# Kernel tuning notes

Hardware: AMD Instinct MI355X
Metric: run time of the kernel (lower is better)

Reference implementation:

```python
import jax, jax.numpy as jnp
import numpy as np

B, T, D_IN, H = 1024, 512, 32, 64


def setup_inputs() -> dict:
    key = jax.random.key(0)
    ks = jax.random.split(key, 16)
    s_in = 1.0 / np.sqrt(H)  # torch LSTM init scale 1/sqrt(hidden)
    inp = {
        "x": jax.random.normal(ks[0], (B, T, D_IN), dtype=jnp.float32),
        # layer 0
        "Wih0": jax.random.uniform(ks[1], (4 * H, D_IN), minval=-s_in, maxval=s_in),
        "Whh0": jax.random.uniform(ks[2], (4 * H, H), minval=-s_in, maxval=s_in),
        "bih0": jax.random.uniform(ks[3], (4 * H,), minval=-s_in, maxval=s_in),
        "bhh0": jax.random.uniform(ks[4], (4 * H,), minval=-s_in, maxval=s_in),
        # layer 1
        "Wih1": jax.random.uniform(ks[5], (4 * H, H), minval=-s_in, maxval=s_in),
        "Whh1": jax.random.uniform(ks[6], (4 * H, H), minval=-s_in, maxval=s_in),
        "bih1": jax.random.uniform(ks[7], (4 * H,), minval=-s_in, maxval=s_in),
        "bhh1": jax.random.uniform(ks[8], (4 * H,), minval=-s_in, maxval=s_in),
        # head: Linear(H, H//2) -> ReLU -> Linear(H//2, 1)
        "W1": jax.random.uniform(ks[9], (H // 2, H), minval=-s_in, maxval=s_in),
        "b1": jax.random.uniform(ks[10], (H // 2,), minval=-s_in, maxval=s_in),
        "W2": jax.random.uniform(ks[11], (1, H // 2), minval=-1.0 / np.sqrt(H // 2), maxval=1.0 / np.sqrt(H // 2)),
        "b2": jax.random.uniform(ks[12], (1,), minval=-1.0 / np.sqrt(H // 2), maxval=1.0 / np.sqrt(H // 2)),
    }
    return inp


def _lstm_layer(x, Wih, Whh, bih, bhh):
    # x: [B, T, D]; returns all hidden states [B, T, H]
    b = x.shape[0]
    xT = jnp.swapaxes(x, 0, 1)  # [T, B, D]
    h0 = jnp.zeros((b, H), dtype=x.dtype)
    c0 = jnp.zeros((b, H), dtype=x.dtype)
    bias = bih + bhh

    def step(carry, xt):
        h, c = carry
        z = xt @ Wih.T + h @ Whh.T + bias  # [B, 4H]
        i, f, g, o = jnp.split(z, 4, axis=-1)  # torch gate order: i, f, g, o
        i = jax.nn.sigmoid(i)
        f = jax.nn.sigmoid(f)
        g = jnp.tanh(g)
        o = jax.nn.sigmoid(o)
        c = f * c + i * g
        h = o * jnp.tanh(c)
        return (h, c), h

    _, hs = jax.lax.scan(step, (h0, c0), xT)
    return jnp.swapaxes(hs, 0, 1)  # [B, T, H]


def reference(x, Wih0, Whh0, bih0, bhh0, Wih1, Whh1, bih1, bhh1, W1, b1, W2, b2):
    h1 = _lstm_layer(x, Wih0, Whh0, bih0, bhh0)   # [B, T, H]
    h2 = _lstm_layer(h1, Wih1, Whh1, bih1, bhh1)  # [B, T, H] (dropout = identity, eval)
    last = h2[:, -1]                              # [B, H]
    hidden = jax.nn.relu(last @ W1.T + b1)        # [B, H//2]
    out = hidden @ W2.T + b2                      # [B, 1]
    return out[:, 0]                              # [B]
```

## Files before the change

kernel.cpp:

```cpp
#include <hip/hip_runtime.h>

#define T       512
#define DIN     32
#define HCELLS  64
#define NB      16
#define NSLICE  64
#define TB      256
#define CH      16
#define NCH     (T / CH)

typedef _Float16 half8  __attribute__((ext_vector_type(8)));
typedef _Float16 half4v __attribute__((ext_vector_type(4)));
typedef float    float4v __attribute__((ext_vector_type(4)));

#define STRH    72
#define SB_HALFS (2*16*STRH)

#define LOG2E   1.44269504f
#define SLOG2E  2.88539008f

#define BARRIER() asm volatile("s_waitcnt lgkmcnt(0)\n\ts_barrier" ::: "memory")

#define WS_FLAG_BYTES 4096
#define H0T   (16 * HCELLS)
#define H0S   ((size_t)T * H0T)
#define WS_NEED (WS_FLAG_BYTES + (size_t)NSLICE * H0S * sizeof(_Float16))

__device__ __forceinline__ int hidx(int p, int n, int k) { return (p * 16 + n) * STRH + k; }

__device__ __forceinline__ void cvt8(const float* v, half8& hi) {
    #pragma unroll
    for (int e = 0; e < 8; ++e) hi[e] = (_Float16)v[e];
}

__device__ __forceinline__ void cell_vec(float4v z0, float4v z1, float4v z2, float4v z3,
                                         float4v& cs, half4v& hh, float4v* hout)
{
    float4v ei, ef, G2, eo, rFP, C2, rOC;
    #pragma unroll
    for (int r = 0; r < 4; ++r) ei[r] = __builtin_amdgcn_exp2f(z0[r]);
    #pragma unroll
    for (int r = 0; r < 4; ++r) ef[r] = __builtin_amdgcn_exp2f(z1[r]);
    #pragma unroll
    for (int r = 0; r < 4; ++r) G2[r] = __builtin_amdgcn_exp2f(z2[r]);
    #pragma unroll
    for (int r = 0; r < 4; ++r) eo[r] = __builtin_amdgcn_exp2f(z3[r]);

    float4v I  = 1.0f + ei;
    float4v F  = 1.0f + ef;
    float4v Gp = 1.0f + G2;
    float4v P  = I * Gp;
    float4v FP = F * P;
    #pragma unroll
    for (int r = 0; r < 4; ++r) rFP[r] = __builtin_amdgcn_rcpf(FP[r]);

    float4v Gms, num, csn;
    #pragma unroll
    for (int r = 0; r < 4; ++r) Gms[r] = fmaf(SLOG2E, G2[r], -SLOG2E);
    #pragma unroll
    for (int r = 0; r < 4; ++r) num[r] = fmaf(F[r], Gms[r], cs[r] * P[r]);
    csn = num * rFP;
    #pragma unroll
    for (int r = 0; r < 4; ++r) csn[r] = fminf(fmaxf(csn[r], -50.0f), 50.0f);
    cs = csn;

    #pragma unroll
    for (int r = 0; r < 4; ++r) C2[r] = __builtin_amdgcn_exp2f(csn[r]);
    float4v O   = 1.0f + eo;
    float4v OCp = O * (1.0f + C2);
    #pragma unroll
    for (int r = 0; r < 4; ++r) rOC[r] = __builtin_amdgcn_rcpf(OCp[r]);
    float4v h = (C2 - 1.0f) * rOC;
    if (hout) *hout = h;
    #pragma unroll
    for (int r = 0; r < 4; ++r) hh[r] = (_Float16)h[r];
}

__global__ void __launch_bounds__(TB, 1)
lstm2_pipe_kernel(const float* __restrict__ x,
                  const float* __restrict__ Wih0, const float* __restrict__ Whh0,
                  const float* __restrict__ bih0, const float* __restrict__ bhh0,
                  const float* __restrict__ Wih1, const float* __restrict__ Whh1,
                  const float* __restrict__ bih1, const float* __restrict__ bhh1,
                  const float* __restrict__ W1,   const float* __restrict__ b1,
                  const float* __restrict__ W2,   const float* __restrict__ b2,
                  unsigned* __restrict__ prog, _Float16* __restrict__ h0g,
                  float* __restrict__ out)
{
    const int tid  = threadIdx.x;
    const int wl   = tid >> 6;
    const int lane = tid & 63;
    const int n16  = lane & 15;
    const int q    = lane >> 4;
    const int j0   = wl * 16 + q * 4;

    const int g     = blockIdx.x;
    const int role  = (g >> 3) & 1;
    const int slice = ((g >> 4) << 3) | (g & 7);
    const int b0    = slice * NB;

    __shared__ __align__(16) _Float16 SB[SB_HALFS];
    __shared__ __align__(16) float HS[16 * 68 + 16 * 33];

    const float gsc[4] = {-LOG2E, -LOG2E, SLOG2E, -LOG2E};

    half8 ah[4][4];
    float4v biasv[4];

    #pragma unroll
    for (int l = 0; l < 4; ++l) {
        const int row = (l * 4 + wl) * 16 + n16;
        const float g2 = gsc[l];
        float v[8];
        if (role == 0) {
            {
                const float4* p = (const float4*)(Wih0 + row * DIN + q * 8);
                float4 u0 = p[0], u1 = p[1];
                v[0]=g2*u0.x; v[1]=g2*u0.y; v[2]=g2*u0.z; v[3]=g2*u0.w;
                v[4]=g2*u1.x; v[5]=g2*u1.y; v[6]=g2*u1.z; v[7]=g2*u1.w;
                cvt8(v, ah[l][0]);
            }
            #pragma unroll
            for (int kt = 1; kt < 3; ++kt) {
                const float4* p = (const float4*)(Whh0 + row * HCELLS + (kt - 1) * 32 + q * 8);
                float4 u0 = p[0], u1 = p[1];
                v[0]=g2*u0.x; v[1]=g2*u0.y; v[2]=g2*u0.z; v[3]=g2*u0.w;
                v[4]=g2*u1.x; v[5]=g2*u1.y; v[6]=g2*u1.z; v[7]=g2*u1.w;
                cvt8(v, ah[l][kt]);
            }
            const int r0 = l * 64 + j0;
            float4v bi = *(const float4v*)(bih0 + r0);
            float4v bh = *(const float4v*)(bhh0 + r0);
            biasv[l] = (bi + bh) * g2;
        } else {
            #pragma unroll
            for (int kt = 0; kt < 4; ++kt) {
                const float* base = (kt < 2) ? (Wih1 + row * HCELLS + kt * 32)
                                             : (Whh1 + row * HCELLS + (kt - 2) * 32);
                const float4* p = (const float4*)(base + q * 8);
                float4 u0 = p[0], u1 = p[1];
                v[0]=g2*u0.x; v[1]=g2*u0.y; v[2]=g2*u0.z; v[3]=g2*u0.w;
                v[4]=g2*u1.x; v[5]=g2*u1.y; v[6]=g2*u1.z; v[7]=g2*u1.w;
                cvt8(v, ah[l][kt]);
            }
            const int r0 = l * 64 + j0;
            float4v bi = *(const float4v*)(bih1 + r0);
            float4v bh = *(const float4v*)(bhh1 + r0);
            biasv[l] = (bi + bh) * g2;
        }
    }

    for (int i = tid; i < SB_HALFS / 2; i += TB) ((int*)SB)[i] = 0;
    __syncthreads();

    float4v cs4 = {0.f, 0.f, 0.f, 0.f};
    float4v hl4;

    if (role == 0) {
        const float* xq = x + ((size_t)(b0 + n16) * T) * DIN + q * 8;
        float4 xn0 = ((const float4*)xq)[0];
        float4 xn1 = ((const float4*)xq)[1];
        xq += DIN;

        _Float16* hstream = h0g + (size_t)slice * H0S + n16 * HCELLS + j0;

        #pragma unroll 2
        for (int t = 0; t < T; ++t) {
            const int pr = t & 1, pw = pr ^ 1;

            float4 xc0 = xn0, xc1 = xn1;
            if (t + 1 < T) { xn0 = ((const float4*)xq)[0]; xn1 = ((const float4*)xq)[1]; xq += DIN; }

            half8 bhx;
            bhx[0]=(_Float16)xc0.x; bhx[1]=(_Float16)xc0.y; bhx[2]=(_Float16)xc0.z; bhx[3]=(_Float16)xc0.w;
            bhx[4]=(_Float16)xc1.x; bhx[5]=(_Float16)xc1.y; bhx[6]=(_Float16)xc1.z; bhx[7]=(_Float16)xc1.w;

            float4v acc[4];
            #pragma unroll
            for (int l = 0; l < 4; ++l)
                acc[l] = __builtin_amdgcn_mfma_f32_16x16x32_f16(ah[l][0], bhx, biasv[l], 0, 0, 0);
            half8 bh0a = *(const half8*)&SB[hidx(pr, n16, q * 8)];
            half8 bh0b = *(const half8*)&SB[hidx(pr, n16, 32 + q * 8)];
            #pragma unroll
            for (int l = 0; l < 4; ++l)
                acc[l] = __builtin_amdgcn_mfma_f32_16x16x32_f16(ah[l][1], bh0a, acc[l], 0, 0, 0);
            #pragma unroll
            for (int l = 0; l < 4; ++l)
                acc[l] = __builtin_amdgcn_mfma_f32_16x16x32_f16(ah[l][2], bh0b, acc[l], 0, 0, 0);

            half4v hh;
            cell_vec(acc[0], acc[1], acc[2], acc[3], cs4, hh, nullptr);
            *(half4v*)&SB[hidx(pw, n16, j0)] = hh;
            *(half4v*)(hstream + (size_t)t * H0T) = hh;

            if ((t & (CH - 1)) == (CH - 1)) {
                __syncthreads();
                if (tid == 0)
                    __hip_atomic_store(prog + slice, (unsigned)(t / CH + 1),
                                       __ATOMIC_RELEASE, __HIP_MEMORY_SCOPE_AGENT);
            } else {
                BARRIER();
            }
        }
        return;
    }

    const _Float16* gbase = h0g + (size_t)slice * H0S + n16 * HCELLS;
    const int ka = q * 8, kb = 32 + q * 8;

    half8 a_cur, b_cur;
    for (int c = 0; c < NCH; ++c) {
        if (tid == 0) {
            unsigned v;
            while ((v = __hip_atomic_load(prog + slice, __ATOMIC_ACQUIRE,
                                          __HIP_MEMORY_SCOPE_AGENT)) < (unsigned)(c + 1))
                __builtin_amdgcn_s_sleep(2);
        }
        __syncthreads();

        {
            const _Float16* p0 = gbase + (size_t)(c * CH) * H0T;
            a_cur = *(const half8*)(p0 + ka);
            b_cur = *(const half8*)(p0 + kb);
        }

        #pragma unroll 2
        for (int i = 0; i < CH; ++i) {
            const int t = c * CH + i;
            const int sr = (i + 1) & 1;
            const int sw = i & 1;

            half8 a_nxt, b_nxt;
            if (i + 1 < CH) {
                const _Float16* pn = gbase + (size_t)(t + 1) * H0T;
                a_nxt = *(const half8*)(pn + ka);
                b_nxt = *(const half8*)(pn + kb);
            }

            float4v acc[4];
            #pragma unroll
            for (int l = 0; l < 4; ++l)
                acc[l] = __builtin_amdgcn_mfma_f32_16x16x32_f16(ah[l][0], a_cur, biasv[l], 0, 0, 0);
            #pragma unroll
            for (int l = 0; l < 4; ++l)
                acc[l] = __builtin_amdgcn_mfma_f32_16x16x32_f16(ah[l][1], b_cur, acc[l], 0, 0, 0);
            half8 c1 = *(const half8*)&SB[hidx(sr, n16, q * 8)];
            half8 c2 = *(const half8*)&SB[hidx(sr, n16, 32 + q * 8)];
            #pragma unroll
            for (int l = 0; l < 4; ++l)
                acc[l] = __builtin_amdgcn_mfma_f32_16x16x32_f16(ah[l][2], c1, acc[l], 0, 0, 0);
            #pragma unroll
            for (int l = 0; l < 4; ++l)
                acc[l] = __builtin_amdgcn_mfma_f32_16x16x32_f16(ah[l][3], c2, acc[l], 0, 0, 0);

            half4v hh;
            cell_vec(acc[0], acc[1], acc[2], acc[3], cs4, hh, &hl4);
            *(half4v*)&SB[hidx(sw, n16, j0)] = hh;
            BARRIER();

            a_cur = a_nxt; b_cur = b_nxt;
        }
    }

    float* h1f = HS;
    float* hid = HS + 16 * 68;
    *(float4v*)&h1f[n16 * 68 + j0] = hl4;
    __syncthreads();

    {
        const int n2 = tid >> 4, m = tid & 15;
        float s0 = b1[m], s1 = b1[m + 16];
        const float* w0p = W1 + m * HCELLS;
        const float* w1p = W1 + (m + 16) * HCELLS;
        #pragma unroll
        for (int j = 0; j < HCELLS; ++j) {
            float hv = h1f[n2 * 68 + j];
            s0 = fmaf(w0p[j], hv, s0);
            s1 = fmaf(w1p[j], hv, s1);
        }
        hid[n2 * 33 + m]      = fmaxf(s0, 0.0f);
        hid[n2 * 33 + m + 16] = fmaxf(s1, 0.0f);
    }
    __syncthreads();

    if (tid < NB) {
        float s = b2[0];
        #pragma unroll
        for (int m = 0; m < 32; ++m) s = fmaf(W2[m], hid[tid * 33 + m], s);
        out[b0 + tid] = s;
    }
}

#define TBF     512
#define FB_H0   0
#define FB_H1   (2*16*STRH)
#define FB_HALFS (FB_H1 + 2*16*STRH)

__device__ __forceinline__ void cell_update(const float4v acc[4], float* cs,
                                            half4v& hh, float* hout)
{
    #pragma unroll
    for (int r = 0; r < 4; ++r) {
        float ei = __builtin_amdgcn_exp2f(acc[0][r]);
        float ef = __builtin_amdgcn_exp2f(acc[1][r]);
        float G2 = __builtin_amdgcn_exp2f(acc[2][r]);
        float I  = 1.0f + ei, F = 1.0f + ef;
        float Gp = 1.0f + G2;
        float Gms = fmaf(SLOG2E, G2, -SLOG2E);
        float P   = I * Gp;
        float num = fmaf(F, Gms, cs[r] * P);
        float csn = num * __builtin_amdgcn_rcpf(F * P);
        csn = fminf(fmaxf(csn, -50.0f), 50.0f);
        cs[r] = csn;
        float eo = __builtin_amdgcn_exp2f(acc[3][r]);
        float C2 = __builtin_amdgcn_exp2f(csn);
        float O  = 1.0f + eo;
        float Cp = 1.0f + C2, Cm = C2 - 1.0f;
        float h  = Cm * __builtin_amdgcn_rcpf(O * Cp);
        if (hout) hout[r] = h;
        hh[r] = (_Float16)h;
    }
}

__global__ void __launch_bounds__(TBF, 2)
lstm2_mfma_fallback(const float* __restrict__ x,
                    const float* __restrict__ Wih0, const float* __restrict__ Whh0,
                    const float* __restrict__ bih0, const float* __restrict__ bhh0,
                    const float* __restrict__ Wih1, const float* __restrict__ Whh1,
                    const float* __restrict__ bih1, const float* __restrict__ bhh1,
                    const float* __restrict__ W1,   const float* __restrict__ b1,
                    const float* __restrict__ W2,   const float* __restrict__ b2,
                    float* __restrict__ out)
{
    const int tid  = threadIdx.x;
    const int wid  = tid >> 6;
    const int grp  = wid >> 2;
    const int wl   = wid & 3;
    const int lane = tid & 63;
    const int n16  = lane & 15;
    const int q    = lane >> 4;
    const int j0   = wl * 16 + q * 4;
    const int b0   = blockIdx.x * NB;

    __shared__ __align__(16) _Float16 SB[FB_HALFS];
    __shared__ __align__(16) float HS[16 * 68 + 16 * 33];

    const float gsc[4] = {-LOG2E, -LOG2E, SLOG2E, -LOG2E};
    half8 ah[4][4];
    float4v biasv[4];

    #pragma unroll
    for (int l = 0; l < 4; ++l) {
        const int row = (l * 4 + wl) * 16 + n16;
        const float g = gsc[l];
        float v[8];
        if (grp == 0) {
            {
                const float4* p = (const float4*)(Wih0 + row * DIN + q * 8);
                float4 u0 = p[0], u1 = p[1];
                v[0]=g*u0.x; v[1]=g*u0.y; v[2]=g*u0.z; v[3]=g*u0.w;
                v[4]=g*u1.x; v[5]=g*u1.y; v[6]=g*u1.z; v[7]=g*u1.w;
                cvt8(v, ah[l][0]);
            }
            #pragma unroll
            for (int kt = 1; kt < 3; ++kt) {
                const float4* p = (const float4*)(Whh0 + row * HCELLS + (kt - 1) * 32 + q * 8);
                float4 u0 = p[0], u1 = p[1];
                v[0]=g*u0.x; v[1]=g*u0.y; v[2]=g*u0.z; v[3]=g*u0.w;
                v[4]=g*u1.x; v[5]=g*u1.y; v[6]=g*u1.z; v[7]=g*u1.w;
                cvt8(v, ah[l][kt]);
            }
            const int r0 = l * 64 + j0;
            float4v bi = *(const float4v*)(bih0 + r0);
            float4v bh = *(const float4v*)(bhh0 + r0);
            biasv[l] = (bi + bh) * g;
        } else {
            #pragma unroll
            for (int kt = 0; kt < 4; ++kt) {
                const float* base = (kt < 2) ? (Wih1 + row * HCELLS + kt * 32)
                                             : (Whh1 + row * HCELLS + (kt - 2) * 32);
                const float4* p = (const float4*)(base + q * 8);
                float4 u0 = p[0], u1 = p[1];
                v[0]=g*u0.x; v[1]=g*u0.y; v[2]=g*u0.z; v[3]=g*u0.w;
                v[4]=g*u1.x; v[5]=g*u1.y; v[6]=g*u1.z; v[7]=g*u1.w;
                cvt8(v, ah[l][kt]);
            }
            const int r0 = l * 64 + j0;
            float4v bi = *(const float4v*)(bih1 + r0);
            float4v bh = *(const float4v*)(bhh1 + r0);
            biasv[l] = (bi + bh) * g;
        }
    }

    for (int i = tid; i < FB_HALFS / 2; i += TBF) ((int*)SB)[i] = 0;

    const float* xq = nullptr;
    float4 xn0, xn1;
    if (grp == 0) {
        xq = x + ((size_t)(b0 + n16) * T) * DIN + q * 8;
        xn0 = *(const float4*)xq;
        xn1 = *(const float4*)(xq + 4);
        xq += DIN;
    }
    __syncthreads();

    float cs[4] = {0, 0, 0, 0};
    float hlast[4];

    #pragma unroll 2
    for (int t = 0; t < T; ++t) {
        const int pr = t & 1, pw = pr ^ 1;
        if (grp == 0) {
            float4 xc0 = xn0, xc1 = xn1;
            if (t + 1 < T) { xn0 = *(const float4*)xq; xn1 = *(const float4*)(xq + 4); xq += DIN; }
            half8 bhx;
            bhx[0]=(_Float16)xc0.x; bhx[1]=(_Float16)xc0.y; bhx[2]=(_Float16)xc0.z; bhx[3]=(_Float16)xc0.w;
            bhx[4]=(_Float16)xc1.x; bhx[5]=(_Float16)xc1.y; bhx[6]=(_Float16)xc1.z; bhx[7]=(_Float16)xc1.w;
            float4v acc[4];
            #pragma unroll
            for (int l = 0; l < 4; ++l)
                acc[l] = __builtin_amdgcn_mfma_f32_16x16x32_f16(ah[l][0], bhx, biasv[l], 0, 0, 0);
            #pragma unroll
            for (int kt = 1; kt < 3; ++kt) {
                half8 bh = *(const half8*)&SB[FB_H0 + hidx(pr, n16, (kt - 1) * 32 + q * 8)];
                #pragma unroll
                for (int l = 0; l < 4; ++l)
                    acc[l] = __builtin_amdgcn_mfma_f32_16x16x32_f16(ah[l][kt], bh, acc[l], 0, 0, 0);
            }
            half4v hh;
            cell_update(acc, cs, hh, nullptr);
            *(half4v*)&SB[FB_H0 + hidx(pw, n16, j0)] = hh;
        } else if (t > 0) {
            float4v acc[4];
            #pragma unroll
            for (int l = 0; l < 4; ++l) acc[l] = biasv[l];
            #pragma unroll
            for (int kt = 0; kt < 4; ++kt) {
                half8 bh = (kt < 2)
                    ? *(const half8*)&SB[FB_H0 + hidx(pr, n16, kt * 32 + q * 8)]
                    : *(const half8*)&SB[FB_H1 + hidx(pw, n16, (kt - 2) * 32 + q * 8)];
                #pragma unroll
                for (int l = 0; l < 4; ++l)
                    acc[l] = __builtin_amdgcn_mfma_f32_16x16x32_f16(ah[l][kt], bh, acc[l], 0, 0, 0);
            }
            half4v hh;
            cell_update(acc, cs, hh, nullptr);
            *(half4v*)&SB[FB_H1 + hidx(pr, n16, j0)] = hh;
        }
        BARRIER();
    }

    float* h1f = HS;
    float* hid = HS + 16 * 68;
    if (grp == 1) {
        float4v acc[4];
        #pragma unroll
        for (int l = 0; l < 4; ++l) acc[l] = biasv[l];
        #pragma unroll
        for (int kt = 0; kt < 4; ++kt) {
            half8 bh = (kt < 2)
                ? *(const half8*)&SB[FB_H0 + hidx(0, n16, kt * 32 + q * 8)]
                : *(const half8*)&SB[FB_H1 + hidx(1, n16, (kt - 2) * 32 + q * 8)];
            #pragma unroll
            for (int l = 0; l < 4; ++l)
                acc[l] = __builtin_amdgcn_mfma_f32_16x16x32_f16(ah[l][kt], bh, acc[l], 0, 0, 0);
        }
        half4v hh;
        cell_update(acc, cs, hh, hlast);
        *(float4*)&h1f[n16 * 68 + j0] = *(const float4*)hlast;
    }
    __syncthreads();

    if (tid < 256) {
        const int n2 = tid >> 4, m = tid & 15;
        float s0 = b1[m], s1 = b1[m + 16];
        const float* w0p = W1 + m * HCELLS;
        const float* w1p = W1 + (m + 16) * HCELLS;
        #pragma unroll
        for (int j = 0; j < HCELLS; ++j) {
            float hv = h1f[n2 * 68 + j];
            s0 = fmaf(w0p[j], hv, s0);
            s1 = fmaf(w1p[j], hv, s1);
        }
        hid[n2 * 33 + m]      = fmaxf(s0, 0.0f);
        hid[n2 * 33 + m + 16] = fmaxf(s1, 0.0f);
    }
    __syncthreads();

    if (tid < NB) {
        float s = b2[0];
        #pragma unroll
        for (int m = 0; m < 32; ++m) s = fmaf(W2[m], hid[tid * 33 + m], s);
        out[b0 + tid] = s;
    }
}

extern "C" void kernel_launch(void* const* d_in, const int* in_sizes, int n_in,
                              void* d_out, int out_size, void* d_ws, size_t ws_size,
                              hipStream_t stream) {
    const float* x    = (const float*)d_in[0];
    const float* Wih0 = (const float*)d_in[1];
    const float* Whh0 = (const float*)d_in[2];
    const float* bih0 = (const float*)d_in[3];
    const float* bhh0 = (const float*)d_in[4];
    const float* Wih1 = (const float*)d_in[5];
    const float* Whh1 = (const float*)d_in[6];
    const float* bih1 = (const float*)d_in[7];
    const float* bhh1 = (const float*)d_in[8];
    const float* W1   = (const float*)d_in[9];
    const float* b1   = (const float*)d_in[10];
    const float* W2   = (const float*)d_in[11];
    const float* b2   = (const float*)d_in[12];
    float* out = (float*)d_out;

    if (d_ws != nullptr && ws_size >= WS_NEED) {
        hipMemsetAsync(d_ws, 0, WS_FLAG_BYTES, stream);
        unsigned*  prog = (unsigned*)d_ws;
        _Float16*  h0g  = (_Float16*)((char*)d_ws + WS_FLAG_BYTES);
        hipLaunchKernelGGL(lstm2_pipe_kernel, dim3(2 * NSLICE), dim3(TB), 0, stream,
                           x, Wih0, Whh0, bih0, bhh0, Wih1, Whh1, bih1, bhh1,
                           W1, b1, W2, b2, prog, h0g, out);
    } else {
        hipLaunchKernelGGL(lstm2_mfma_fallback, dim3(NSLICE), dim3(TBF), 0, stream,
                           x, Wih0, Whh0, bih0, bhh0, Wih1, Whh1, bih1, bhh1,
                           W1, b1, W2, b2, out);
    }
}
```

Measured before the change: 446.8 us.

## Replace per-step workgroup barriers with LDS flag spin-waits and deepen x prefetch

Each wave now posts a per-wave step counter in LDS after writing its hidden-state slice. Before reading the shared hidden state it spins until all four waves have reached that step, instead of hitting an s_barrier every timestep. The flag wait sits after the input-projection MFMAs, so that work can overlap with waiting on slower waves. The layer-0 x loads are also prefetched two steps ahead instead of one. The risks are LDS polling traffic, subtle ordering correctness with relaxed atomics on the double-buffered LDS, and spin overhead that may cost more than a hardware barrier.

After: 408.6 us. -8.5%, faster.

```diff
diff --git a/kernel.cpp b/kernel.cpp
--- a/kernel.cpp
+++ b/kernel.cpp
@@ -20,6 +20,23 @@
 #define SLOG2E  2.88539008f
 
 #define BARRIER() asm volatile("s_waitcnt lgkmcnt(0)\n\ts_barrier" ::: "memory")
+
+#define FLAG_POST(val) do { \
+    asm volatile("s_waitcnt lgkmcnt(0)" ::: "memory"); \
+    __hip_atomic_store(&FL[wl], (val), __ATOMIC_RELAXED, __HIP_MEMORY_SCOPE_WORKGROUP); \
+} while (0)
+
+#define FLAG_WAIT(need) do { \
+    for (;;) { \
+        int f0_ = __hip_atomic_load(&FL[0], __ATOMIC_RELAXED, __HIP_MEMORY_SCOPE_WORKGROUP); \
+        int f1_ = __hip_atomic_load(&FL[1], __ATOMIC_RELAXED, __HIP_MEMORY_SCOPE_WORKGROUP); \
+        int f2_ = __hip_atomic_load(&FL[2], __ATOMIC_RELAXED, __HIP_MEMORY_SCOPE_WORKGROUP); \
+        int f3_ = __hip_atomic_load(&FL[3], __ATOMIC_RELAXED, __HIP_MEMORY_SCOPE_WORKGROUP); \
+        if (f0_ >= (need) && f1_ >= (need) && f2_ >= (need) && f3_ >= (need)) break; \
+    } \
+    asm volatile("s_waitcnt lgkmcnt(0)" ::: "memory"); \
+    __builtin_amdgcn_sched_barrier(0); \
+} while (0)
 
 #define WS_FLAG_BYTES 4096
 #define H0T   (16 * HCELLS)
@@ -101,6 +118,7 @@
 
     __shared__ __align__(16) _Float16 SB[SB_HALFS];
     __shared__ __align__(16) float HS[16 * 68 + 16 * 33];
+    __shared__ int FL[4];
 
     const float gsc[4] = {-LOG2E, -LOG2E, SLOG2E, -LOG2E};
 
@@ -151,6 +169,7 @@
     }
 
     for (int i = tid; i < SB_HALFS / 2; i += TB) ((int*)SB)[i] = 0;
+    if (tid < 4) FL[tid] = 0;
     __syncthreads();
 
     float4v cs4 = {0.f, 0.f, 0.f, 0.f};
@@ -160,7 +179,9 @@
         const float* xq = x + ((size_t)(b0 + n16) * T) * DIN + q * 8;
         float4 xn0 = ((const float4*)xq)[0];
         float4 xn1 = ((const float4*)xq)[1];
-        xq += DIN;
+        float4 xm0 = ((const float4*)(xq + DIN))[0];
+        float4 xm1 = ((const float4*)(xq + DIN))[1];
+        xq += 2 * DIN;
 
         _Float16* hstream = h0g + (size_t)slice * H0S + n16 * HCELLS + j0;
 
@@ -169,7 +190,8 @@
             const int pr = t & 1, pw = pr ^ 1;
 
             float4 xc0 = xn0, xc1 = xn1;
-            if (t + 1 < T) { xn0 = ((const float4*)xq)[0]; xn1 = ((const float4*)xq)[1]; xq += DIN; }
+            xn0 = xm0; xn1 = xm1;
+            if (t + 2 < T) { xm0 = ((const float4*)xq)[0]; xm1 = ((const float4*)xq)[1]; xq += DIN; }
 
             half8 bhx;
             bhx[0]=(_Float16)xc0.x; bhx[1]=(_Float16)xc0.y; bhx[2]=(_Float16)xc0.z; bhx[3]=(_Float16)xc0.w;
@@ -179,6 +201,9 @@
             #pragma unroll
             for (int l = 0; l < 4; ++l)
                 acc[l] = __builtin_amdgcn_mfma_f32_16x16x32_f16(ah[l][0], bhx, biasv[l], 0, 0, 0);
+
+            FLAG_WAIT(t);
+
             half8 bh0a = *(const half8*)&SB[hidx(pr, n16, q * 8)];
             half8 bh0b = *(const half8*)&SB[hidx(pr, n16, 32 + q * 8)];
             #pragma unroll
@@ -192,14 +217,14 @@
             cell_vec(acc[0], acc[1], acc[2], acc[3], cs4, hh, nullptr);
             *(half4v*)&SB[hidx(pw, n16, j0)] = hh;
             *(half4v*)(hstream + (size_t)t * H0T) = hh;
+
+            FLAG_POST(t + 1);
 
             if ((t & (CH - 1)) == (CH - 1)) {
                 __syncthreads();
                 if (tid == 0)
                     __hip_atomic_store(prog + slice, (unsigned)(t / CH + 1),
                                        __ATOMIC_RELEASE, __HIP_MEMORY_SCOPE_AGENT);
-            } else {
-                BARRIER();
             }
         }
         return;
@@ -244,6 +269,9 @@
             #pragma unroll
             for (int l = 0; l < 4; ++l)
                 acc[l] = __builtin_amdgcn_mfma_f32_16x16x32_f16(ah[l][1], b_cur, acc[l], 0, 0, 0);
+
+            FLAG_WAIT(t);
+
             half8 c1 = *(const half8*)&SB[hidx(sr, n16, q * 8)];
             half8 c2 = *(const half8*)&SB[hidx(sr, n16, 32 + q * 8)];
             #pragma unroll
@@ -256,7 +284,8 @@
             half4v hh;
             cell_vec(acc[0], acc[1], acc[2], acc[3], cs4, hh, &hl4);
             *(half4v*)&SB[hidx(sw, n16, j0)] = hh;
-            BARRIER();
+
+            FLAG_POST(t + 1);
 
             a_cur = a_nxt; b_cur = b_nxt;
         }
```
